# Kernel tuning notes

Hardware: AMD Instinct MI355X
Metric: run time of the kernel (lower is better)

## Reference

```python
import math
import jax, jax.numpy as jnp
import numpy as np

SAMPLE_RATE = 24000
HARMONIC_NUM = 8
SINE_AMP = 0.1


def setup_inputs() -> dict:
    key = jax.random.key(0)
    k1, k2, k3 = jax.random.split(key, 3)
    f0 = jax.random.uniform(k1, (32, 800), dtype=jnp.float32)  # frame-rate F0
    W = jax.random.normal(k2, (9, 1), dtype=jnp.float32) * (1.0 / 3.0)  # Linear(9,1) weight
    b = jax.random.normal(k3, (1,), dtype=jnp.float32) * 0.01
    return {"f0": f0, "W": W, "b": b, "upp": 240}


def reference(f0, W, b, upp):
    # nearest-neighbor upsample by integer factor upp == repeat each frame
    f0_up = jnp.repeat(f0, upp, axis=1)  # [batch, samples]
    batch, samples = f0_up.shape
    # harmonic multipliers h = 1..harmonic_num+1 (9 harmonics)
    h = jnp.arange(1, HARMONIC_NUM + 2, dtype=f0.dtype)  # [9]
    # cumsum(f0_up * h) == cumsum(f0_up) * h (cumsum is linear); one scan for all harmonics
    base_phase = jnp.cumsum(f0_up / SAMPLE_RATE, axis=1)  # [batch, samples]
    phase = base_phase[:, :, None] * (h * (2.0 * math.pi))  # [batch, samples, 9]
    sine = jnp.sin(phase) * SINE_AMP
    uv = (f0_up > 0).astype(f0.dtype)[:, :, None]  # [batch, samples, 1]
    harmonics = sine * uv
    har_source = jnp.tanh(harmonics @ W + b)  # [batch, samples, 1]
    noise = jax.random.normal(jax.random.key(1234), (batch, samples, 1), dtype=f0.dtype) * (SINE_AMP / 3.0)
    return (har_source, noise, uv)
```

## Files before the change

### kernel.cpp

```cpp
#include <hip/hip_runtime.h>
#include <stdint.h>

#define FRAMES  800
#define UPP     240
#define SAMPLES (FRAMES * UPP)
#define BATCH   32
#define NTOT    (BATCH * SAMPLES)

__device__ __forceinline__ uint32_t rotl32(uint32_t v, int d) {
  return (v << d) | (v >> (32 - d));
}

__device__ __forceinline__ void threefry2x32(uint32_t k0, uint32_t k1,
                                             uint32_t x0, uint32_t x1,
                                             uint32_t& o0, uint32_t& o1) {
  const uint32_t ks0 = k0, ks1 = k1, ks2 = k0 ^ k1 ^ 0x1BD11BDAu;
  x0 += ks0; x1 += ks1;
#define TF_R(r) { x0 += x1; x1 = rotl32(x1, r); x1 ^= x0; }
  TF_R(13) TF_R(15) TF_R(26) TF_R(6)   x0 += ks1; x1 += ks2 + 1u;
  TF_R(17) TF_R(29) TF_R(16) TF_R(24)  x0 += ks2; x1 += ks0 + 2u;
  TF_R(13) TF_R(15) TF_R(26) TF_R(6)   x0 += ks0; x1 += ks1 + 3u;
  TF_R(17) TF_R(29) TF_R(16) TF_R(24)  x0 += ks1; x1 += ks2 + 4u;
  TF_R(13) TF_R(15) TF_R(26) TF_R(6)   x0 += ks2; x1 += ks0 + 5u;
#undef TF_R
  o0 = x0; o1 = x1;
}

__device__ __forceinline__ float erfinv_f32(float x) {
  float w = -log1pf(-x * x);
  float p;
  if (w < 5.0f) {
    w = w - 2.5f;
    p = 2.81022636e-08f;
    p = fmaf(p, w, 3.43273939e-07f);
    p = fmaf(p, w, -3.5233877e-06f);
    p = fmaf(p, w, -4.39150654e-06f);
    p = fmaf(p, w, 0.00021858087f);
    p = fmaf(p, w, -0.00125372503f);
    p = fmaf(p, w, -0.00417768164f);
    p = fmaf(p, w, 0.246640727f);
    p = fmaf(p, w, 1.50140941f);
  } else {
    w = sqrtf(w) - 3.0f;
    p = -0.000200214257f;
    p = fmaf(p, w, 0.000100950558f);
    p = fmaf(p, w, 0.00134934322f);
    p = fmaf(p, w, -0.00367342844f);
    p = fmaf(p, w, 0.00573950773f);
    p = fmaf(p, w, -0.0076224613f);
    p = fmaf(p, w, 0.00943887047f);
    p = fmaf(p, w, 1.00167406f);
    p = fmaf(p, w, 2.83297682f);
  }
  return p * x;
}

__device__ __forceinline__ float bits_to_noise(uint32_t bits) {
  float f = __uint_as_float((bits >> 9) | 0x3f800000u);
  float u = f - 1.0f;
  const float lo = -0.99999994f;
  float val = fmaf(u, 2.0f, lo);
  val = fmaxf(lo, val);
  float n = 1.41421356f * erfinv_f32(val);
  return n * 0.033333335f;
}

__device__ __forceinline__ float fast_tanhf(float x) {
  float e = __expf(-2.0f * x);
  return (1.0f - e) * __builtin_amdgcn_rcpf(1.0f + e);
}

__global__ __launch_bounds__(256) void scan_kernel(
    const float* __restrict__ f0, float* __restrict__ pfrac) {
  __shared__ double sScan[256];
  const int tid = threadIdx.x;
  const int row = blockIdx.x;
  const float* f0row = f0 + row * FRAMES;

  const int fb = tid * 4;
  double v0 = 0.0, v1 = 0.0, v2 = 0.0, v3 = 0.0;
  if (fb < FRAMES) {
    v0 = (double)f0row[fb];     v1 = (double)f0row[fb + 1];
    v2 = (double)f0row[fb + 2]; v3 = (double)f0row[fb + 3];
  }
  sScan[tid] = v0 + v1 + v2 + v3;
  __syncthreads();
  for (int off = 1; off < 256; off <<= 1) {
    double add = (tid >= off) ? sScan[tid - off] : 0.0;
    __syncthreads();
    sScan[tid] += add;
    __syncthreads();
  }
  if (fb < FRAMES) {
    const double excl = (tid > 0) ? sScan[tid - 1] : 0.0;
    double p0 = excl;
    double p1 = excl + v0;
    double p2 = excl + v0 + v1;
    double p3 = excl + v0 + v1 + v2;
    float* o = pfrac + row * FRAMES + fb;
    double c0 = p0 * 0.01; o[0] = (float)(c0 - floor(c0));
    double c1 = p1 * 0.01; o[1] = (float)(c1 - floor(c1));
    double c2 = p2 * 0.01; o[2] = (float)(c2 - floor(c2));
    double c3 = p3 * 0.01; o[3] = (float)(c3 - floor(c3));
  }
}

__global__ __launch_bounds__(256) void fused_kernel(
    const float* __restrict__ f0, const float* __restrict__ pfrac,
    const float* __restrict__ W, const float* __restrict__ bptr,
    float* __restrict__ out) {
  const int t0 = (blockIdx.x * 256 + threadIdx.x) * 4;
  if (t0 >= SAMPLES) return;
  const int row = blockIdx.y;

  const int frame = t0 / UPP;
  const int j = t0 - frame * UPP;
  const float fv   = f0[row * FRAMES + frame];
  const float pf   = pfrac[row * FRAMES + frame];
  const float step = fv * (1.0f / 24000.0f);
  const float amp  = (fv > 0.0f) ? 0.1f : 0.0f;
  const float uvf  = (fv > 0.0f) ? 1.0f : 0.0f;

  float Wr[9];
#pragma unroll
  for (int h = 0; h < 9; ++h) Wr[h] = W[h];
  const float bias = bptr[0];

  const uint32_t gbase = (uint32_t)(row * SAMPLES + t0);

  float4 hv, nv;
  float* hvp = &hv.x;
  float* nvp = &nv.x;
#pragma unroll
  for (int k = 0; k < 4; ++k) {
    float ph = fmaf((float)(j + 1 + k), step, pf);
    ph -= (ph >= 1.0f) ? 1.0f : 0.0f;
    float s1 = __builtin_amdgcn_sinf(ph);
    float c1 = __builtin_amdgcn_cosf(ph);
    float tc = 2.0f * c1;
    float skm1 = 0.0f, sk = s1;
    float dot = Wr[0] * s1;
#pragma unroll
    for (int h = 2; h <= 9; ++h) {
      float sn = tc * sk - skm1;
      skm1 = sk; sk = sn;
      dot = fmaf(Wr[h - 1], sn, dot);
    }
    hvp[k] = fast_tanhf(fmaf(amp, dot, bias));

    uint32_t a, b;
    threefry2x32(0u, 1234u, 0u, gbase + (uint32_t)k, a, b);
    nvp[k] = bits_to_noise(a ^ b);
  }

  float* har   = out;
  float* noise = out + NTOT;
  float* uvp   = out + 2 * NTOT;
  *(float4*)(har + gbase)   = hv;
  *(float4*)(noise + gbase) = nv;
  *(float4*)(uvp + gbase)   = make_float4(uvf, uvf, uvf, uvf);
}

extern "C" void kernel_launch(void* const* d_in, const int* in_sizes, int n_in,
                              void* d_out, int out_size, void* d_ws, size_t ws_size,
                              hipStream_t stream) {
  const float* f0 = (const float*)d_in[0];
  const float* W  = (const float*)d_in[1];
  const float* b  = (const float*)d_in[2];

  float* pfrac = (float*)d_ws;
  float* out   = (float*)d_out;

  scan_kernel<<<BATCH, 256, 0, stream>>>(f0, pfrac);
  dim3 g((SAMPLES + 1023) / 1024, BATCH);
  fused_kernel<<<g, 256, 0, stream>>>(f0, pfrac, W, b, out);
}
```

Measured before the change: 113.2 us.

## Fuse phase prefix scan into main kernel via per-block redundant prefix sums

Removes the separate scan kernel and its workspace round-trip. Each block now has one wavefront sum in double precision all frames before the block's first sample, then each thread adds up to five further frames to get its own phase offset. This saves a kernel launch and the serialization between the two kernels. In exchange every block redundantly reads up to 800 floats and performs double-precision adds.

```diff
diff --git a/kernel.cpp b/kernel.cpp
--- a/kernel.cpp
+++ b/kernel.cpp
@@ -70,53 +70,42 @@
   return (1.0f - e) * __builtin_amdgcn_rcpf(1.0f + e);
 }
 
-__global__ __launch_bounds__(256) void scan_kernel(
-    const float* __restrict__ f0, float* __restrict__ pfrac) {
-  __shared__ double sScan[256];
-  const int tid = threadIdx.x;
-  const int row = blockIdx.x;
+__global__ __launch_bounds__(256) void fused_kernel(
+    const float* __restrict__ f0, const float* __restrict__ W,
+    const float* __restrict__ bptr, float* __restrict__ out) {
+  const int row = blockIdx.y;
   const float* f0row = f0 + row * FRAMES;
 
-  const int fb = tid * 4;
-  double v0 = 0.0, v1 = 0.0, v2 = 0.0, v3 = 0.0;
-  if (fb < FRAMES) {
-    v0 = (double)f0row[fb];     v1 = (double)f0row[fb + 1];
-    v2 = (double)f0row[fb + 2]; v3 = (double)f0row[fb + 3];
+  const int blockSample0 = blockIdx.x * 1024;
+  const int Fb = blockSample0 / UPP;
+
+  __shared__ double sBase;
+  if (threadIdx.x < 64) {
+    double p = 0.0;
+    for (int i = threadIdx.x; i < Fb; i += 64) p += (double)f0row[i];
+#pragma unroll
+    for (int off = 32; off > 0; off >>= 1) p += __shfl_xor(p, off, 64);
+    if (threadIdx.x == 0) sBase = p;
   }
-  sScan[tid] = v0 + v1 + v2 + v3;
   __syncthreads();
-  for (int off = 1; off < 256; off <<= 1) {
-    double add = (tid >= off) ? sScan[tid - off] : 0.0;
-    __syncthreads();
-    sScan[tid] += add;
-    __syncthreads();
-  }
-  if (fb < FRAMES) {
-    const double excl = (tid > 0) ? sScan[tid - 1] : 0.0;
-    double p0 = excl;
-    double p1 = excl + v0;
-    double p2 = excl + v0 + v1;
-    double p3 = excl + v0 + v1 + v2;
-    float* o = pfrac + row * FRAMES + fb;
-    double c0 = p0 * 0.01; o[0] = (float)(c0 - floor(c0));
-    double c1 = p1 * 0.01; o[1] = (float)(c1 - floor(c1));
-    double c2 = p2 * 0.01; o[2] = (float)(c2 - floor(c2));
-    double c3 = p3 * 0.01; o[3] = (float)(c3 - floor(c3));
-  }
-}
 
-__global__ __launch_bounds__(256) void fused_kernel(
-    const float* __restrict__ f0, const float* __restrict__ pfrac,
-    const float* __restrict__ W, const float* __restrict__ bptr,
-    float* __restrict__ out) {
-  const int t0 = (blockIdx.x * 256 + threadIdx.x) * 4;
+  const int t0 = blockSample0 + (int)threadIdx.x * 4;
   if (t0 >= SAMPLES) return;
-  const int row = blockIdx.y;
 
   const int frame = t0 / UPP;
+  double prefix = sBase;
+#pragma unroll
+  for (int i = 0; i < 5; ++i) {
+    int idx = Fb + i;
+    int idxc = (idx < FRAMES - 1) ? idx : (FRAMES - 1);
+    double v = (double)f0row[idxc];
+    prefix += (idx < frame) ? v : 0.0;
+  }
+  double c = prefix * 0.01;
+  const float pf = (float)(c - floor(c));
+
   const int j = t0 - frame * UPP;
-  const float fv   = f0[row * FRAMES + frame];
-  const float pf   = pfrac[row * FRAMES + frame];
+  const float fv   = f0row[frame];
   const float step = fv * (1.0f / 24000.0f);
   const float amp  = (fv > 0.0f) ? 0.1f : 0.0f;
   const float uvf  = (fv > 0.0f) ? 1.0f : 0.0f;
@@ -167,11 +156,9 @@
   const float* f0 = (const float*)d_in[0];
   const float* W  = (const float*)d_in[1];
   const float* b  = (const float*)d_in[2];
+  (void)d_ws; (void)ws_size;
 
-  float* pfrac = (float*)d_ws;
-  float* out   = (float*)d_out;
-
-  scan_kernel<<<BATCH, 256, 0, stream>>>(f0, pfrac);
+  float* out = (float*)d_out;
   dim3 g((SAMPLES + 1023) / 1024, BATCH);
-  fused_kernel<<<g, 256, 0, stream>>>(f0, pfrac, W, b, out);
+  fused_kernel<<<g, 256, 0, stream>>>(f0, W, b, out);
 }
```

New measurement: 111.8 us. No clear change (-1.2%).
